# Kernel optimization log

Measured on AMD Instinct MI355X. Metric: run time of the kernel, lower is better.

The kernel has to match this reference:

```python
import jax, jax.numpy as jnp
import numpy as np

N = 100000      # nodes
E = 1600000     # edges (avg degree 16)
IN = 256        # input feature dim
HID = 64        # per-head hidden dim
H = 4           # attention heads
FC = 256        # collator dim (= H*HID here)
OUT = 4         # classes
ALPHA = 0.2     # LeakyReLU slope


def setup_inputs() -> dict:
    key = jax.random.key(0)
    ks = jax.random.split(key, 24)

    def rn(k, shape, fan_in):
        return jax.random.normal(k, shape, jnp.float32) / np.sqrt(fan_in).astype(np.float32)

    x = jax.random.normal(ks[0], (N, IN), jnp.float32)
    # ensure every node appears at least once as a source so the softmax denom is nonzero
    src = jnp.concatenate([jnp.arange(N, dtype=jnp.int32),
                           jax.random.randint(ks[1], (E - N,), 0, N, dtype=jnp.int32)])
    dst = jax.random.randint(ks[2], (E,), 0, N, dtype=jnp.int32)
    edge_index = jnp.stack([src, dst], axis=0)  # [2, E]

    # layer 1 heads (conv1d k=1 == linear): W [H, HID, IN]; a_1/a_2 conv -> vectors + scalar bias
    W1 = rn(ks[3], (H, HID, IN), IN)
    a11_w = rn(ks[4], (H, HID), HID); a11_b = jnp.zeros((H,), jnp.float32)
    a12_w = rn(ks[5], (H, HID), HID); a12_b = jnp.zeros((H,), jnp.float32)
    b1 = jnp.zeros((H, HID), jnp.float32)
    # layer 2 heads: input is H*HID
    W2 = rn(ks[6], (H, HID, H * HID), H * HID)
    a21_w = rn(ks[7], (H, HID), HID); a21_b = jnp.zeros((H,), jnp.float32)
    a22_w = rn(ks[8], (H, HID), HID); a22_b = jnp.zeros((H,), jnp.float32)
    b2 = jnp.zeros((H, HID), jnp.float32)
    # collator + classifier
    Wc = rn(ks[9], (FC, H * HID), H * HID); bc = jnp.zeros((FC,), jnp.float32)
    Wcls = rn(ks[10], (OUT, FC), FC); bcls = jnp.zeros((OUT,), jnp.float32)

    return dict(x=x, edge_index=edge_index,
                W1=W1, a11_w=a11_w, a11_b=a11_b, a12_w=a12_w, a12_b=a12_b, b1=b1,
                W2=W2, a21_w=a21_w, a21_b=a21_b, a22_w=a22_w, a22_b=a22_b, b2=b2,
                Wc=Wc, bc=bc, Wcls=Wcls, bcls=bcls)


def _gat_head(x, src, dst, W, a1w, a1b, a2w, a2b, b):
    h = x @ W.T                              # [N, HID]
    a1 = h @ a1w + a1b                       # [N] per-node src score
    a2 = h @ a2w + a2b                       # [N] per-node dst score
    s = jnp.exp(jax.nn.leaky_relu(a1[src] + a2[dst], ALPHA))   # [E]
    denom = jax.ops.segment_sum(s, src, num_segments=N)        # [N]
    agg = jax.ops.segment_sum(s[:, None] * h[dst], src, num_segments=N)  # [N, HID]
    return agg / denom[:, None] + b


def reference(x, edge_index, W1, a11_w, a11_b, a12_w, a12_b, b1,
              W2, a21_w, a21_b, a22_w, a22_b, b2, Wc, bc, Wcls, bcls):
    src, dst = edge_index[0], edge_index[1]
    h1 = jnp.concatenate(
        [_gat_head(x, src, dst, W1[i], a11_w[i], a11_b[i], a12_w[i], a12_b[i], b1[i])
         for i in range(H)], axis=1)         # [N, H*HID]
    h1 = jax.nn.relu(h1)
    h2 = jnp.concatenate(
        [_gat_head(h1, src, dst, W2[i], a21_w[i], a21_b[i], a22_w[i], a22_b[i], b2[i])
         for i in range(H)], axis=1)         # [N, H*HID]
    feat = jax.nn.relu(h2 @ Wc.T + bc)       # [N, FC]
    return feat @ Wcls.T + bcls              # [N, OUT]
```

## Files before the change

### kernel.cpp

```cpp
#include <hip/hip_runtime.h>
#include <hip/hip_bf16.h>
#include <hip/hip_fp16.h>
#include <stdint.h>

#define H 4
#define HID 64
#define CDIM 256
#define OUTC 4
#define ALPHA 0.2f
#define NW 16
#define MAXB 512
#define TILE1 4096

typedef __attribute__((ext_vector_type(8))) _Float16 f16x8;
typedef __attribute__((ext_vector_type(4))) float f32x4;

#define GLOBAL_AS(p) ((const __attribute__((address_space(1))) void*)(p))
#define LDS_AS(p)    ((__attribute__((address_space(3))) void*)(p))

__global__ void detect_k(const uint32_t* __restrict__ xw, int* __restrict__ flag) {
    __shared__ int sd[256];
    int t = threadIdx.x;
    int hits = 0;
    for (int i = 0; i < 16; ++i) {
        uint32_t w = xw[t * 16 + i];
        uint32_t ex = (w >> 7) & 0xffu;
        if (ex >= 100u && ex <= 145u) hits++;
    }
    sd[t] = hits;
    __syncthreads();
    for (int s = 128; s > 0; s >>= 1) {
        if (t < s) sd[t] += sd[t + s];
        __syncthreads();
    }
    if (t == 0) *flag = (sd[0] > 3000) ? 1 : 0;
}

struct WPtrs {
    const void* p[NW];
    int sz[NW];
    int off[NW];
};

__global__ void convert_k(WPtrs ptrs, float* __restrict__ outf, __half* __restrict__ outh,
                          const int* __restrict__ flag) {
    int which = blockIdx.y;
    int n = ptrs.sz[which];
    int i = blockIdx.x * 256 + threadIdx.x;
    if (i >= n) return;
    float v;
    if (*flag) v = __bfloat162float(((const __hip_bfloat16*)ptrs.p[which])[i]);
    else       v = ((const float*)ptrs.p[which])[i];
    outf[ptrs.off[which] + i] = v;
    outh[ptrs.off[which] + i] = __float2half(v);
}

__global__ __launch_bounds__(512) void bhist_k(const int* __restrict__ srcI,
                                               int* __restrict__ bucketCnt,
                                               int Ee, int nbuck)
{
    __shared__ int bc[MAXB];
    int t = threadIdx.x;
    bc[t] = 0;
    __syncthreads();
    int base = blockIdx.x * TILE1;
    #pragma unroll
    for (int q = 0; q < 8; ++q) {
        int i = base + q * 512 + t;
        if (i < Ee) atomicAdd(&bc[srcI[i] >> 8], 1);
    }
    __syncthreads();
    if (t < nbuck && bc[t] > 0) atomicAdd(&bucketCnt[t], bc[t]);
}

__global__ __launch_bounds__(512) void bscan_k(
    const int* __restrict__ bucketCnt, int* __restrict__ bucketCur,
    int* __restrict__ bucketStart, int* __restrict__ rowStart,
    int nbuck, int Nn, int Ee)
{
    __shared__ int sd[MAXB];
    int t = threadIdx.x;
    int v = (t < nbuck) ? bucketCnt[t] : 0;
    sd[t] = v;
    __syncthreads();
    for (int off = 1; off < MAXB; off <<= 1) {
        int add = (t >= off) ? sd[t - off] : 0;
        __syncthreads();
        sd[t] += add;
        __syncthreads();
    }
    if (t < nbuck) {
        int excl = sd[t] - v;
        bucketCur[t] = excl;
        bucketStart[t] = excl;
    }
    if (t == 0) { bucketStart[nbuck] = Ee; rowStart[Nn] = Ee; }
}

__global__ __launch_bounds__(512) void pass1_k(
    const int* __restrict__ srcI, const int* __restrict__ dstI,
    int* __restrict__ bucketCur, uint32_t* __restrict__ pairs,
    int Ee, int nbuck)
{
    __shared__ int cntL[MAXB], scanL[MAXB], exclL[MAXB], curL[MAXB], gbaseL[MAXB];
    __shared__ uint32_t sortedV[TILE1];
    __shared__ uint16_t sortedB[TILE1];
    const int t = threadIdx.x;
    const int base = blockIdx.x * TILE1;
    cntL[t] = 0;
    __syncthreads();
    uint32_t vq[8]; int bq[8];
    #pragma unroll
    for (int q = 0; q < 8; ++q) {
        int i = base + q * 512 + t;
        if (i < Ee) {
            int s = srcI[i], d = dstI[i];
            bq[q] = s >> 8;
            vq[q] = ((uint32_t)d << 8) | (uint32_t)(s & 255);
            atomicAdd(&cntL[bq[q]], 1);
        } else bq[q] = -1;
    }
    __syncthreads();
    scanL[t] = cntL[t];
    __syncthreads();
    for (int off = 1; off < MAXB; off <<= 1) {
        int add = (t >= off) ? scanL[t - off] : 0;
        __syncthreads();
        scanL[t] += add;
        __syncthreads();
    }
    int excl = scanL[t] - cntL[t];
    exclL[t] = excl;
    curL[t] = excl;
    if (t < nbuck && cntL[t] > 0)
        gbaseL[t] = atomicAdd(&bucketCur[t], cntL[t]);
    __syncthreads();
    #pragma unroll
    for (int q = 0; q < 8; ++q) {
        if (bq[q] >= 0) {
            int pos = atomicAdd(&curL[bq[q]], 1);
            sortedV[pos] = vq[q];
            sortedB[pos] = (uint16_t)bq[q];
        }
    }
    __syncthreads();
    int tcount = min(TILE1, Ee - base);
    for (int j = t; j < tcount; j += 512) {
        int b = sortedB[j];
        pairs[gbaseL[b] + (j - exclL[b])] = sortedV[j];
    }
}

__global__ __launch_bounds__(256) void pass2_k(
    const uint32_t* __restrict__ pairs, const int* __restrict__ bucketStart,
    int* __restrict__ rowStart, int* __restrict__ colI, int Nn)
{
    __shared__ int ncnt[256], sd[256], lcur[256];
    int b = blockIdx.x, t = threadIdx.x;
    int n0 = b << 8;
    int s = bucketStart[b], e = bucketStart[b + 1];
    ncnt[t] = 0;
    __syncthreads();
    for (int p = s + t; p < e; p += 256)
        atomicAdd(&ncnt[pairs[p] & 255], 1);
    __syncthreads();
    int v = ncnt[t];
    sd[t] = v;
    __syncthreads();
    for (int off = 1; off < 256; off <<= 1) {
        int add = (t >= off) ? sd[t - off] : 0;
        __syncthreads();
        sd[t] += add;
        __syncthreads();
    }
    int start = s + sd[t] - v;
    lcur[t] = start;
    if (n0 + t < Nn) rowStart[n0 + t] = start;
    __syncthreads();
    for (int p = s + t; p < e; p += 256) {
        uint32_t pv = pairs[p];
        int q = atomicAdd(&lcur[pv & 255], 1);
        colI[q] = (int)(pv >> 8);
    }
}

template <int AMODE, int OMODE>
__global__ __launch_bounds__(256) void gemm_k(
    const void* __restrict__ Ap, const __half* __restrict__ B,
    const float* __restrict__ bias, void* __restrict__ Cp, int M,
    const int* __restrict__ flagp,
    const float* __restrict__ a1w, const float* __restrict__ a1b,
    const float* __restrict__ a2w, const float* __restrict__ a2b,
    float* __restrict__ a1v, __half* __restrict__ a2v)
{
    __shared__ __align__(16) char smem[128 * 136 * 2];
    const int tid  = threadIdx.x;
    int r, cblk;
    {
        const int bid = blockIdx.x;
        const int nrow = gridDim.x >> 1;
        const int nfull16 = (nrow >> 3) << 4;
        if (bid < nfull16) { r = (bid >> 4) * 8 + (bid & 7); cblk = (bid >> 3) & 1; }
        else { int t2 = bid - nfull16; r = (nfull16 >> 1) + (t2 >> 1); cblk = t2 & 1; }
    }
    const int row0 = r * 128;
    const int col0 = cblk * 128;
    const int wave = tid >> 6, lane = tid & 63;
    const int m0w = (wave & 1) * 64;
    const int n0w = (wave >> 1) * 64;
    const int lm = lane & 15, lg = lane >> 4;
    const int isbf = (AMODE == 0) ? *flagp : 0;

    const __half* A = (const __half*)Ap;
    const int lrow = wave * 32 + (lane >> 2);
    const int kcL  = lane & 3;
    const size_t arow0 = (size_t)min(row0 + lrow,      M - 1) * CDIM;
    const size_t arow1 = (size_t)min(row0 + lrow + 16, M - 1) * CDIM;
    const size_t brow0 = (size_t)(col0 + lrow) * CDIM;
    const size_t brow1 = (size_t)(col0 + lrow + 16) * CDIM;

    f32x4 acc[4][4] = {};

    auto stageAB = [&](int buf, int k0) {
        char* Ab = smem + buf * 16384;
        char* Bb = Ab + 8192;
        if constexpr (AMODE == 1) {
            __builtin_amdgcn_global_load_lds(GLOBAL_AS(A + arow0 + k0 + kcL * 8),
                LDS_AS(Ab + wave * 2048), 16, 0, 0);
            __builtin_amdgcn_global_load_lds(GLOBAL_AS(A + arow1 + k0 + kcL * 8),
                LDS_AS(Ab + wave * 2048 + 1024), 16, 0, 0);
        } else {
            #pragma unroll
            for (int l = 0; l < 2; ++l) {
                int c = tid + l * 256;
                int m = c >> 2, kc = c & 3;
                int gr = row0 + m;
                uint4 q = make_uint4(0u, 0u, 0u, 0u);
                if (gr < M) {
                    __half hv[8];
                    if (isbf) {
                        const uint4 qb = *(const uint4*)((const __hip_bfloat16*)Ap
                                           + (size_t)gr * CDIM + k0 + kc * 8);
                        const uint32_t* w = (const uint32_t*)&qb;
                        #pragma unroll
                        for (int p = 0; p < 4; ++p) {
                            hv[2*p]   = __float2half(__uint_as_float((w[p] & 0xffffu) << 16));
                            hv[2*p+1] = __float2half(__uint_as_float(w[p] & 0xffff0000u));
                        }
                    } else {
                        const float* Af = (const float*)Ap + (size_t)gr * CDIM + k0 + kc * 8;
                        const float4 f0 = *(const float4*)Af;
                        const float4 f1 = *(const float4*)(Af + 4);
                        hv[0]=__float2half(f0.x); hv[1]=__float2half(f0.y);
                        hv[2]=__float2half(f0.z); hv[3]=__float2half(f0.w);
                        hv[4]=__float2half(f1.x); hv[5]=__float2half(f1.y);
                        hv[6]=__float2half(f1.z); hv[7]=__float2half(f1.w);
                    }
                    q = *(uint4*)hv;
                }
                *(uint4*)(Ab + m * 64 + kc * 16) = q;
            }
        }
        __builtin_amdgcn_global_load_lds(GLOBAL_AS(B + brow0 + k0 + kcL * 8),
            LDS_AS(Bb + wave * 2048), 16, 0, 0);
        __builtin_amdgcn_global_load_lds(GLOBAL_AS(B + brow1 + k0 + kcL * 8),
            LDS_AS(Bb + wave * 2048 + 1024), 16, 0, 0);
    };

    stageAB(0, 0);
    if constexpr (AMODE == 0) __syncthreads();
    int cur = 0;
    for (int kt = 0; kt < 8; ++kt) {
        if (kt < 7) stageAB(cur ^ 1, (kt + 1) * 32);
        if constexpr (AMODE == 1) {
            if (kt < 7) asm volatile("s_waitcnt vmcnt(4)" ::: "memory");
            else        asm volatile("s_waitcnt vmcnt(0)" ::: "memory");
            __builtin_amdgcn_s_barrier();
            asm volatile("" ::: "memory");
            __builtin_amdgcn_sched_barrier(0);
        } else {
            __syncthreads();
        }
        const char* Ab = smem + cur * 16384;
        const char* Bb = Ab + 8192;
        f16x8 af[4], bfr[4];
        #pragma unroll
        for (int i = 0; i < 4; ++i)
            af[i] = *(const f16x8*)(Ab + (m0w + i * 16 + lm) * 64 + lg * 16);
        #pragma unroll
        for (int j = 0; j < 4; ++j)
            bfr[j] = *(const f16x8*)(Bb + (n0w + j * 16 + lm) * 64 + lg * 16);
        #pragma unroll
        for (int i = 0; i < 4; ++i)
            #pragma unroll
            for (int j = 0; j < 4; ++j)
                acc[i][j] = __builtin_amdgcn_mfma_f32_16x16x32_f16(
                    af[i], bfr[j], acc[i][j], 0, 0, 0);
        if constexpr (AMODE == 1) {
            __builtin_amdgcn_sched_barrier(0);
            asm volatile("" ::: "memory");
            __builtin_amdgcn_s_barrier();
            asm volatile("" ::: "memory");
        } else {
            __syncthreads();
        }
        cur ^= 1;
    }

    if constexpr (OMODE == 1) {
        __half (*Cs)[136] = (__half(*)[136])smem;
        #pragma unroll
        for (int i = 0; i < 4; ++i)
            #pragma unroll
            for (int r2 = 0; r2 < 4; ++r2) {
                int lr = m0w + i * 16 + lg * 4 + r2;
                #pragma unroll
                for (int j = 0; j < 4; ++j)
                    Cs[lr][n0w + j * 16 + lm] = __float2half(acc[i][j][r2]);
            }
        __syncthreads();
        __half* C = (__half*)Cp;
        #pragma unroll
        for (int l = 0; l < 8; ++l) {
            int c = tid + l * 256;
            int rr = c >> 4, cc = c & 15;
            int gr = row0 + rr;
            if (gr < M)
                *(uint4*)(C + (size_t)gr * CDIM + col0 + cc * 8) = *(uint4*)(&Cs[rr][cc * 8]);
        }
        {
            const int hsel = wave >> 1;
            const int ghead = (col0 >> 6) + hsel;
            float wv1[4], wv2[4];
            #pragma unroll
            for (int j = 0; j < 4; ++j) {
                wv1[j] = a1w[ghead * 64 + j * 16 + lm];
                wv2[j] = a2w[ghead * 64 + j * 16 + lm];
            }
            const float b1s = a1b[ghead], b2s = a2b[ghead];
            #pragma unroll
            for (int i = 0; i < 4; ++i)
                #pragma unroll
                for (int r2 = 0; r2 < 4; ++r2) {
                    float p1 = 0.f, p2 = 0.f;
                    #pragma unroll
                    for (int j = 0; j < 4; ++j) {
                        float v = acc[i][j][r2];
                        p1 = fmaf(v, wv1[j], p1);
                        p2 = fmaf(v, wv2[j], p2);
                    }
                    #pragma unroll
                    for (int m = 1; m < 16; m <<= 1) {
                        p1 += __shfl_xor(p1, m);
                        p2 += __shfl_xor(p2, m);
                    }
                    int gr = row0 + m0w + i * 16 + lg * 4 + r2;
                    if (lm == 0 && gr < M) {
                        a1v[(size_t)gr * H + ghead] = p1 + b1s;
                        a2v[(size_t)gr * H + ghead] = __float2half(p2 + b2s);
                    }
                }
        }
    } else {
        const float* Wc4 = a1w;
        float* pcls = a1v;
        const int slot = cblk * 2 + (wave >> 1);
        float wv[OUTC][4];
        #pragma unroll
        for (int o = 0; o < OUTC; ++o)
            #pragma unroll
            for (int j = 0; j < 4; ++j)
                wv[o][j] = Wc4[o * CDIM + col0 + n0w + j * 16 + lm];
        #pragma unroll
        for (int i = 0; i < 4; ++i)
            #pragma unroll
            for (int r2 = 0; r2 < 4; ++r2) {
                int grow = row0 + m0w + i * 16 + lg * 4 + r2;
                if (grow < M) {
                    float po[OUTC] = {0.f, 0.f, 0.f, 0.f};
                    #pragma unroll
                    for (int j = 0; j < 4; ++j) {
                        int gcol = col0 + n0w + j * 16 + lm;
                        float t = fmaxf(acc[i][j][r2] + bias[gcol], 0.f);
                        #pragma unroll
                        for (int o = 0; o < OUTC; ++o)
                            po[o] = fmaf(t, wv[o][j], po[o]);
                    }
                    #pragma unroll
                    for (int m = 1; m < 16; m <<= 1)
                        #pragma unroll
                        for (int o = 0; o < OUTC; ++o)
                            po[o] += __shfl_xor(po[o], m);
                    if (lm < OUTC) {
                        float v = (lm == 0) ? po[0] : (lm == 1) ? po[1]
                                : (lm == 2) ? po[2] : po[3];
                        pcls[((size_t)grow * 4 + slot) * OUTC + lm] = v;
                    }
                }
            }
        (void)Cp;
    }
}

__global__ __launch_bounds__(256) void agg_k(
    const __half* __restrict__ h,
    const float* __restrict__ a1v, const __half* __restrict__ a2v,
    const int* __restrict__ rowStart, const int* __restrict__ colI,
    const float* __restrict__ bias, __half* __restrict__ outp, int relu, int Nn)
{
    int tid = threadIdx.x;
    int wave = tid >> 6, lane = tid & 63;
    int n = blockIdx.x * 4 + wave;
    if (n >= Nn) return;
    int head = lane >> 4;
    int s = rowStart[n], e = rowStart[n + 1];
    float ac0 = 0.f, ac1 = 0.f, ac2 = 0.f, ac3 = 0.f, den = 0.f;
    const __half* hl = h + lane * 4;
    const float a1n = a1v[(size_t)n * H + head];

    for (int p0 = s; p0 < e; p0 += 8) {
        const int cnt = e - p0;
        int d[8]; float a2q[8]; ushort4 u[8];
        #pragma unroll
        for (int q = 0; q < 8; ++q) {
            int p = p0 + ((q < cnt) ? q : 0);
            d[q] = colI[p];
        }
        #pragma unroll
        for (int q = 0; q < 8; ++q) {
            u[q] = *(const ushort4*)(hl + (size_t)d[q] * CDIM);
            a2q[q] = __half2float(a2v[(size_t)d[q] * H + head]);
        }
        #pragma unroll
        for (int q = 0; q < 8; ++q) {
            float z = a1n + a2q[q];
            z = (z > 0.f) ? z : ALPHA * z;
            float svq = (q < cnt) ? __expf(z) : 0.f;
            den += svq;
            ac0 = fmaf(svq, __half2float(__ushort_as_half(u[q].x)), ac0);
            ac1 = fmaf(svq, __half2float(__ushort_as_half(u[q].y)), ac1);
            ac2 = fmaf(svq, __half2float(__ushort_as_half(u[q].z)), ac2);
            ac3 = fmaf(svq, __half2float(__ushort_as_half(u[q].w)), ac3);
        }
    }

    den = (den > 0.f) ? den : 1.f;
    const float4 b4 = *(const float4*)(bias + lane * 4);
    float r0 = ac0 / den + b4.x;
    float r1 = ac1 / den + b4.y;
    float r2 = ac2 / den + b4.z;
    float r3 = ac3 / den + b4.w;
    if (relu) {
        r0 = fmaxf(r0, 0.f); r1 = fmaxf(r1, 0.f);
        r2 = fmaxf(r2, 0.f); r3 = fmaxf(r3, 0.f);
    }
    ushort4 o;
    o.x = __half_as_ushort(__float2half(r0));
    o.y = __half_as_ushort(__float2half(r1));
    o.z = __half_as_ushort(__float2half(r2));
    o.w = __half_as_ushort(__float2half(r3));
    *(ushort4*)(outp + (size_t)n * CDIM + lane * 4) = o;
}

__global__ void cls2_k(const float* __restrict__ pcls, const float* __restrict__ bcls,
                       void* __restrict__ out, int Nn, const int* __restrict__ flagp)
{
    int n = blockIdx.x * 256 + threadIdx.x;
    if (n >= Nn) return;
    const float4 p0 = *(const float4*)(pcls + (size_t)n * 16);
    const float4 p1 = *(const float4*)(pcls + (size_t)n * 16 + 4);
    const float4 p2 = *(const float4*)(pcls + (size_t)n * 16 + 8);
    const float4 p3 = *(const float4*)(pcls + (size_t)n * 16 + 12);
    float r0 = p0.x + p1.x + p2.x + p3.x + bcls[0];
    float r1 = p0.y + p1.y + p2.y + p3.y + bcls[1];
    float r2 = p0.z + p1.z + p2.z + p3.z + bcls[2];
    float r3 = p0.w + p1.w + p2.w + p3.w + bcls[3];
    if (*flagp) {
        __hip_bfloat16* o = (__hip_bfloat16*)out + (size_t)n * OUTC;
        o[0] = __float2bfloat16(r0); o[1] = __float2bfloat16(r1);
        o[2] = __float2bfloat16(r2); o[3] = __float2bfloat16(r3);
    } else {
        float* o = (float*)out + (size_t)n * OUTC;
        o[0] = r0; o[1] = r1; o[2] = r2; o[3] = r3;
    }
}

extern "C" void kernel_launch(void* const* d_in, const int* in_sizes, int n_in,
                              void* d_out, int out_size, void* d_ws, size_t ws_size,
                              hipStream_t stream)
{
    const void* x  = d_in[0];
    const int*  ei = (const int*)d_in[1];

    const int Nn = in_sizes[0] / CDIM;
    const int Ee = in_sizes[1] / 2;
    const int* srcI = ei;
    const int* dstI = ei + Ee;

    char* wsp = (char*)d_ws;
    size_t off = 0;
    auto alloc = [&](size_t bytes) -> void* {
        void* p = wsp + off;
        off += (bytes + 255) & ~(size_t)255;
        return p;
    };
    __half* hA   = (__half*)alloc((size_t)Nn * CDIM * 2);
    __half* hB   = (__half*)alloc((size_t)Nn * CDIM * 2);
    float*  a1v       = (float*)alloc((size_t)Nn * H * 4);
    __half* a2h       = (__half*)alloc((size_t)Nn * H * 2);
    float*  pcls      = (float*)alloc((size_t)Nn * 4 * OUTC * 4);
    int*    rowStart  = (int*)alloc((size_t)(Nn + 1) * 4);
    int*    colI      = (int*)alloc((size_t)Ee * 4);
    uint32_t* pairs   = (uint32_t*)alloc((size_t)Ee * 4);
    int*    bucketCnt   = (int*)alloc(MAXB * 4);
    int*    bucketCur   = (int*)alloc(MAXB * 4);
    int*    bucketStart = (int*)alloc((MAXB + 1) * 4);
    int*    flag      = (int*)alloc(256);
    float*  wconv     = (float*)alloc((size_t)200000 * 4);
    __half* wh        = (__half*)alloc((size_t)200000 * 2);
    (void)ws_size; (void)n_in; (void)out_size;

    detect_k<<<1, 256, 0, stream>>>((const uint32_t*)x, flag);
    WPtrs wp;
    int woff = 0;
    for (int i = 0; i < NW; ++i) {
        wp.p[i] = d_in[2 + i];
        wp.sz[i] = in_sizes[2 + i];
        wp.off[i] = woff;
        woff += in_sizes[2 + i];
    }
    {
        dim3 cgrid(256, NW);
        convert_k<<<cgrid, 256, 0, stream>>>(wp, wconv, wh, flag);
    }
    const float*  a11wf = wconv + wp.off[1];
    const float*  a11bf = wconv + wp.off[2];
    const float*  a12wf = wconv + wp.off[3];
    const float*  a12bf = wconv + wp.off[4];
    const float*  b1f   = wconv + wp.off[5];
    const float*  a21wf = wconv + wp.off[7];
    const float*  a21bf = wconv + wp.off[8];
    const float*  a22wf = wconv + wp.off[9];
    const float*  a22bf = wconv + wp.off[10];
    const float*  b2f   = wconv + wp.off[11];
    const float*  bcf   = wconv + wp.off[13];
    const float*  Wclsf = wconv + wp.off[14];
    const float*  bclsf = wconv + wp.off[15];
    const __half* W1h   = wh + wp.off[0];
    const __half* W2h   = wh + wp.off[6];
    const __half* Wch   = wh + wp.off[12];

    const int NB = (Nn + 255) / 256;
    const int NBUCK = (Nn + 255) >> 8;
    const int TB = (Ee + TILE1 - 1) / TILE1;

    hipMemsetAsync(bucketCnt, 0, MAXB * 4, stream);
    bhist_k<<<TB, 512, 0, stream>>>(srcI, bucketCnt, Ee, NBUCK);
    bscan_k<<<1, 512, 0, stream>>>(bucketCnt, bucketCur, bucketStart, rowStart,
                                   NBUCK, Nn, Ee);
    pass1_k<<<TB, 512, 0, stream>>>(srcI, dstI, bucketCur, pairs, Ee, NBUCK);
    pass2_k<<<NBUCK, 256, 0, stream>>>(pairs, bucketStart, rowStart, colI, Nn);

    const int NROW = (Nn + 127) / 128;
    dim3 ggrid(NROW * 2);
    const int AB = (Nn + 3) / 4;

    gemm_k<0, 1><<<ggrid, 256, 0, stream>>>(x, W1h, nullptr, hA, Nn, flag,
                                            a11wf, a11bf, a12wf, a12bf, a1v, a2h);
    agg_k<<<AB, 256, 0, stream>>>(hA, a1v, a2h, rowStart, colI, b1f, hB, 1, Nn);

    gemm_k<1, 1><<<ggrid, 256, 0, stream>>>(hB, W2h, nullptr, hA, Nn, flag,
                                            a21wf, a21bf, a22wf, a22bf, a1v, a2h);
    agg_k<<<AB, 256, 0, stream>>>(hA, a1v, a2h, rowStart, colI, b2f, hB, 0, Nn);

    gemm_k<1, 0><<<ggrid, 256, 0, stream>>>(hB, Wch, bcf, nullptr, Nn, flag,
                                            Wclsf, nullptr, nullptr, nullptr,
                                            pcls, nullptr);
    cls2_k<<<NB, 256, 0, stream>>>(pcls, bclsf, d_out, Nn, flag);
}
```

Baseline: 616.1 us.

## Pre-convert x to fp16 and split aggregation into eight chunked launches

```diff
diff --git a/kernel.cpp b/kernel.cpp
--- a/kernel.cpp
+++ b/kernel.cpp
@@ -55,6 +55,32 @@
     outh[ptrs.off[which] + i] = __float2half(v);
 }
 
+__global__ __launch_bounds__(256) void xconv_k(const void* __restrict__ xp,
+                                               __half* __restrict__ xh,
+                                               const int* __restrict__ flag,
+                                               int units ) {
+    int i = blockIdx.x * 256 + threadIdx.x;
+    if (i >= units) return;
+    __half hv[8];
+    if (*flag) {
+        const uint4 qb = *((const uint4*)xp + i);
+        const uint32_t* w = (const uint32_t*)&qb;
+        #pragma unroll
+        for (int p = 0; p < 4; ++p) {
+            hv[2*p]   = __float2half(__uint_as_float((w[p] & 0xffffu) << 16));
+            hv[2*p+1] = __float2half(__uint_as_float(w[p] & 0xffff0000u));
+        }
+    } else {
+        const float4 f0 = *((const float4*)xp + (size_t)i * 2);
+        const float4 f1 = *((const float4*)xp + (size_t)i * 2 + 1);
+        hv[0]=__float2half(f0.x); hv[1]=__float2half(f0.y);
+        hv[2]=__float2half(f0.z); hv[3]=__float2half(f0.w);
+        hv[4]=__float2half(f1.x); hv[5]=__float2half(f1.y);
+        hv[6]=__float2half(f1.z); hv[7]=__float2half(f1.w);
+    }
+    *(uint4*)(xh + (size_t)i * 8) = *(uint4*)hv;
+}
+
 __global__ __launch_bounds__(512) void bhist_k(const int* __restrict__ srcI,
                                                int* __restrict__ bucketCnt,
                                                int Ee, int nbuck)
@@ -184,11 +210,10 @@
     }
 }
 
-template <int AMODE, int OMODE>
+template <int OMODE>
 __global__ __launch_bounds__(256) void gemm_k(
-    const void* __restrict__ Ap, const __half* __restrict__ B,
+    const __half* __restrict__ A, const __half* __restrict__ B,
     const float* __restrict__ bias, void* __restrict__ Cp, int M,
-    const int* __restrict__ flagp,
     const float* __restrict__ a1w, const float* __restrict__ a1b,
     const float* __restrict__ a2w, const float* __restrict__ a2b,
     float* __restrict__ a1v, __half* __restrict__ a2v)
@@ -209,9 +234,7 @@
     const int m0w = (wave & 1) * 64;
     const int n0w = (wave >> 1) * 64;
     const int lm = lane & 15, lg = lane >> 4;
-    const int isbf = (AMODE == 0) ? *flagp : 0;
-
-    const __half* A = (const __half*)Ap;
+
     const int lrow = wave * 32 + (lane >> 2);
     const int kcL  = lane & 3;
     const size_t arow0 = (size_t)min(row0 + lrow,      M - 1) * CDIM;
@@ -224,43 +247,10 @@
     auto stageAB = [&](int buf, int k0) {
         char* Ab = smem + buf * 16384;
         char* Bb = Ab + 8192;
-        if constexpr (AMODE == 1) {
-            __builtin_amdgcn_global_load_lds(GLOBAL_AS(A + arow0 + k0 + kcL * 8),
-                LDS_AS(Ab + wave * 2048), 16, 0, 0);
-            __builtin_amdgcn_global_load_lds(GLOBAL_AS(A + arow1 + k0 + kcL * 8),
-                LDS_AS(Ab + wave * 2048 + 1024), 16, 0, 0);
-        } else {
-            #pragma unroll
-            for (int l = 0; l < 2; ++l) {
-                int c = tid + l * 256;
-                int m = c >> 2, kc = c & 3;
-                int gr = row0 + m;
-                uint4 q = make_uint4(0u, 0u, 0u, 0u);
-                if (gr < M) {
-                    __half hv[8];
-                    if (isbf) {
-                        const uint4 qb = *(const uint4*)((const __hip_bfloat16*)Ap
-                                           + (size_t)gr * CDIM + k0 + kc * 8);
-                        const uint32_t* w = (const uint32_t*)&qb;
-                        #pragma unroll
-                        for (int p = 0; p < 4; ++p) {
-                            hv[2*p]   = __float2half(__uint_as_float((w[p] & 0xffffu) << 16));
-                            hv[2*p+1] = __float2half(__uint_as_float(w[p] & 0xffff0000u));
-                        }
-                    } else {
-                        const float* Af = (const float*)Ap + (size_t)gr * CDIM + k0 + kc * 8;
-                        const float4 f0 = *(const float4*)Af;
-                        const float4 f1 = *(const float4*)(Af + 4);
-                        hv[0]=__float2half(f0.x); hv[1]=__float2half(f0.y);
-                        hv[2]=__float2half(f0.z); hv[3]=__float2half(f0.w);
-                        hv[4]=__float2half(f1.x); hv[5]=__float2half(f1.y);
-                        hv[6]=__float2half(f1.z); hv[7]=__float2half(f1.w);
-                    }
-                    q = *(uint4*)hv;
-                }
-                *(uint4*)(Ab + m * 64 + kc * 16) = q;
-            }
-        }
+        __builtin_amdgcn_global_load_lds(GLOBAL_AS(A + arow0 + k0 + kcL * 8),
+            LDS_AS(Ab + wave * 2048), 16, 0, 0);
+        __builtin_amdgcn_global_load_lds(GLOBAL_AS(A + arow1 + k0 + kcL * 8),
+            LDS_AS(Ab + wave * 2048 + 1024), 16, 0, 0);
         __builtin_amdgcn_global_load_lds(GLOBAL_AS(B + brow0 + k0 + kcL * 8),
             LDS_AS(Bb + wave * 2048), 16, 0, 0);
         __builtin_amdgcn_global_load_lds(GLOBAL_AS(B + brow1 + k0 + kcL * 8),
@@ -268,19 +258,14 @@
     };
 
     stageAB(0, 0);
-    if constexpr (AMODE == 0) __syncthreads();
     int cur = 0;
     for (int kt = 0; kt < 8; ++kt) {
         if (kt < 7) stageAB(cur ^ 1, (kt + 1) * 32);
-        if constexpr (AMODE == 1) {
-            if (kt < 7) asm volatile("s_waitcnt vmcnt(4)" ::: "memory");
-            else        asm volatile("s_waitcnt vmcnt(0)" ::: "memory");
-            __builtin_amdgcn_s_barrier();
-            asm volatile("" ::: "memory");
-            __builtin_amdgcn_sched_barrier(0);
-        } else {
-            __syncthreads();
-        }
+        if (kt < 7) asm volatile("s_waitcnt vmcnt(4)" ::: "memory");
+        else        asm volatile("s_waitcnt vmcnt(0)" ::: "memory");
+        __builtin_amdgcn_s_barrier();
+        asm volatile("" ::: "memory");
+        __builtin_amdgcn_sched_barrier(0);
         const char* Ab = smem + cur * 16384;
         const char* Bb = Ab + 8192;
         f16x8 af[4], bfr[4];
@@ -296,14 +281,10 @@
             for (int j = 0; j < 4; ++j)
                 acc[i][j] = __builtin_amdgcn_mfma_f32_16x16x32_f16(
                     af[i], bfr[j], acc[i][j], 0, 0, 0);
-        if constexpr (AMODE == 1) {
-            __builtin_amdgcn_sched_barrier(0);
-            asm volatile("" ::: "memory");
-            __builtin_amdgcn_s_barrier();
-            asm volatile("" ::: "memory");
-        } else {
-            __syncthreads();
-        }
+        __builtin_amdgcn_sched_barrier(0);
+        asm volatile("" ::: "memory");
+        __builtin_amdgcn_s_barrier();
+        asm volatile("" ::: "memory");
         cur ^= 1;
     }
 
@@ -406,12 +387,13 @@
     const __half* __restrict__ h,
     const float* __restrict__ a1v, const __half* __restrict__ a2v,
     const int* __restrict__ rowStart, const int* __restrict__ colI,
-    const float* __restrict__ bias, __half* __restrict__ outp, int relu, int Nn)
+    const float* __restrict__ bias, __half* __restrict__ outp, int relu,
+    int n0, int n1)
 {
     int tid = threadIdx.x;
     int wave = tid >> 6, lane = tid & 63;
-    int n = blockIdx.x * 4 + wave;
-    if (n >= Nn) return;
+    int n = n0 + blockIdx.x * 4 + wave;
+    if (n >= n1) return;
     int head = lane >> 4;
     int s = rowStart[n], e = rowStart[n + 1];
     float ac0 = 0.f, ac1 = 0.f, ac2 = 0.f, ac3 = 0.f, den = 0.f;
@@ -506,6 +488,7 @@
     };
     __half* hA   = (__half*)alloc((size_t)Nn * CDIM * 2);
     __half* hB   = (__half*)alloc((size_t)Nn * CDIM * 2);
+    __half* xh   = (__half*)alloc((size_t)Nn * CDIM * 2);
     float*  a1v       = (float*)alloc((size_t)Nn * H * 4);
     __half* a2h       = (__half*)alloc((size_t)Nn * H * 2);
     float*  pcls      = (float*)alloc((size_t)Nn * 4 * OUTC * 4);
@@ -554,6 +537,11 @@
     const int NBUCK = (Nn + 255) >> 8;
     const int TB = (Ee + TILE1 - 1) / TILE1;
 
+    {
+        const int units = (Nn * CDIM) / 8;
+        xconv_k<<<(units + 255) / 256, 256, 0, stream>>>(x, xh, flag, units);
+    }
+
     hipMemsetAsync(bucketCnt, 0, MAXB * 4, stream);
     bhist_k<<<TB, 512, 0, stream>>>(srcI, bucketCnt, Ee, NBUCK);
     bscan_k<<<1, 512, 0, stream>>>(bucketCnt, bucketCur, bucketStart, rowStart,
@@ -563,18 +551,29 @@
 
     const int NROW = (Nn + 127) / 128;
     dim3 ggrid(NROW * 2);
-    const int AB = (Nn + 3) / 4;
-
-    gemm_k<0, 1><<<ggrid, 256, 0, stream>>>(x, W1h, nullptr, hA, Nn, flag,
-                                            a11wf, a11bf, a12wf, a12bf, a1v, a2h);
-    agg_k<<<AB, 256, 0, stream>>>(hA, a1v, a2h, rowStart, colI, b1f, hB, 1, Nn);
-
-    gemm_k<1, 1><<<ggrid, 256, 0, stream>>>(hB, W2h, nullptr, hA, Nn, flag,
-                                            a21wf, a21bf, a22wf, a22bf, a1v, a2h);
-    agg_k<<<AB, 256, 0, stream>>>(hA, a1v, a2h, rowStart, colI, b2f, hB, 0, Nn);
-
-    gemm_k<1, 0><<<ggrid, 256, 0, stream>>>(hB, Wch, bcf, nullptr, Nn, flag,
-                                            Wclsf, nullptr, nullptr, nullptr,
-                                            pcls, nullptr);
+    const int CHUNK = (Nn + 7) / 8;
+    const int ABC = (CHUNK + 3) / 4;
+
+    gemm_k<1><<<ggrid, 256, 0, stream>>>(xh, W1h, nullptr, hA, Nn,
+                                         a11wf, a11bf, a12wf, a12bf, a1v, a2h);
+    for (int k = 0; k < 8; ++k) {
+        int n0 = k * CHUNK;
+        if (n0 >= Nn) break;
+        int n1 = min(n0 + CHUNK, Nn);
+        agg_k<<<ABC, 256, 0, stream>>>(hA, a1v, a2h, rowStart, colI, b1f, hB, 1, n0, n1);
+    }
+
+    gemm_k<1><<<ggrid, 256, 0, stream>>>(hB, W2h, nullptr, hA, Nn,
+                                         a21wf, a21bf, a22wf, a22bf, a1v, a2h);
+    for (int k = 0; k < 8; ++k) {
+        int n0 = k * CHUNK;
+        if (n0 >= Nn) break;
+        int n1 = min(n0 + CHUNK, Nn);
+        agg_k<<<ABC, 256, 0, stream>>>(hA, a1v, a2h, rowStart, colI, b2f, hB, 0, n0, n1);
+    }
+
+    gemm_k<0><<<ggrid, 256, 0, stream>>>(hB, Wch, bcf, nullptr, Nn,
+                                         Wclsf, nullptr, nullptr, nullptr,
+                                         pcls, nullptr);
     cls2_k<<<NB, 256, 0, stream>>>(pcls, bclsf, d_out, Nn, flag);
 }
```

After: 680.8 us. 10.5% more time.
